# Kernel optimization log

Hardware: AMD Instinct MI355X
Metric: run time of the kernel (lower is better)

Reference implementation:

```python
import jax, jax.numpy as jnp
import numpy as np

T = 8192   # sequence length (sent_len)
D = 512    # word_emb_dim
H = 2048   # enc_lstm_dim
S = 512    # number of segments (len(action_pos))
EPS = 1e-4 # additive constant in the original _masked_softmax denominator


def setup_inputs() -> dict:
    key = jax.random.key(0)
    ks = jax.random.split(key, 16)
    s = 0.02  # small init scale keeps exp() stable
    seg_len = T // S
    action_pos = (jnp.arange(1, S + 1, dtype=jnp.int32) * seg_len - 1)  # last = T-1
    action = jnp.zeros((T,), jnp.int32).at[action_pos].set(1)
    return {
        "sent": jax.random.normal(ks[0], (T, D), jnp.float32),
        "Wi1": jax.random.normal(ks[1], (3 * H, D), jnp.float32) * s,
        "Wh1": jax.random.normal(ks[2], (3 * H, H), jnp.float32) * s,
        "bi1": jax.random.normal(ks[3], (3 * H,), jnp.float32) * s,
        "bh1": jax.random.normal(ks[4], (3 * H,), jnp.float32) * s,
        "Wi2": jax.random.normal(ks[5], (3 * H, H), jnp.float32) * s,
        "Wh2": jax.random.normal(ks[6], (3 * H, H), jnp.float32) * s,
        "bi2": jax.random.normal(ks[7], (3 * H,), jnp.float32) * s,
        "bh2": jax.random.normal(ks[8], (3 * H,), jnp.float32) * s,
        "Wl": jax.random.normal(ks[9], (H, H), jnp.float32) * s,
        "bl": jax.random.normal(ks[10], (H,), jnp.float32) * s,
        "wa": jax.random.normal(ks[11], (H,), jnp.float32) * s,
        "Wl2": jax.random.normal(ks[12], (H, H), jnp.float32) * s,
        "bl2": jax.random.normal(ks[13], (H,), jnp.float32) * s,
        "wa2": jax.random.normal(ks[14], (H,), jnp.float32) * s,
        "action": action,
        "action_pos": action_pos,
    }


def _gru_scan(xs, reset, Wi, Wh, bi, bh):
    """GRU over leading axis; hidden state zeroed after steps where reset==1.
    xs: (N, in), reset: (N,) int. Returns outputs (N, H)."""
    gi_all = xs @ Wi.T + bi  # (N, 3H) precompute input gates as one GEMM

    def step(h, inp):
        gi, a = inp
        gh = Wh @ h + bh
        r = jax.nn.sigmoid(gi[:H] + gh[:H])
        z = jax.nn.sigmoid(gi[H:2 * H] + gh[H:2 * H])
        n = jnp.tanh(gi[2 * H:] + r * gh[2 * H:])
        hn = (1.0 - z) * n + z * h
        h_next = jnp.where(a == 1, jnp.zeros_like(hn), hn)
        return h_next, hn

    h0 = jnp.zeros((H,), xs.dtype)
    _, outs = jax.lax.scan(step, h0, (gi_all, reset))
    return outs


def _degenerate_softmax(a):
    # Original sums exp over a size-1 axis: w = exp(a) / (exp(a) + 1e-4)
    e = jnp.exp(a)
    return e / (e + EPS)


def reference(sent, Wi1, Wh1, bi1, bh1, Wi2, Wh2, bi2, bh2,
              Wl, bl, wa, Wl2, bl2, wa2, action, action_pos):
    # lower GRU with per-step state reset
    outs = _gru_scan(sent, action, Wi1, Wh1, bi1, bh1)          # (T, H)
    emb_h = jnp.tanh(outs @ Wl.T + bl)                           # (T, H)
    w = _degenerate_softmax(emb_h @ wa)                          # (T,)
    weighted = w[:, None] * emb_h                                # (T, H)
    # segment i covers tokens (action_pos[i-1], action_pos[i]]
    seg_id = jnp.searchsorted(action_pos, jnp.arange(T), side='left')
    seg = jax.ops.segment_max(weighted, seg_id, num_segments=S)  # (S, H)
    # upper GRU over segment embeddings (no resets, zero init)
    outs2 = _gru_scan(seg, jnp.zeros((S,), jnp.int32), Wi2, Wh2, bi2, bh2)
    e2 = jnp.tanh(outs2 @ Wl2.T + bl2)                           # (S, H)
    w2 = _degenerate_softmax(e2 @ wa2)                           # (S,)
    emb = jnp.max(w2[:, None] * e2, axis=0, keepdims=True)       # (1, H)
    return emb
```

## Files before the change

kernel.cpp:

```cpp
#include <hip/hip_runtime.h>
#include <stdint.h>

typedef unsigned short u16;
typedef unsigned int u32;
typedef unsigned long long u64;
typedef __attribute__((ext_vector_type(4))) float f32x4;
typedef __attribute__((ext_vector_type(8))) short bf16x8;

constexpr int kT = 8192;
constexpr int kD = 512;
constexpr int kH = 2048;
constexpr int kH3 = 6144;
constexpr int kS = 512;
constexpr int kSeg = 16;
constexpr int kNWG2 = 256;
constexpr int kREP = 8;

__device__ __forceinline__ float bf2f(u16 u) {
  union { float f; u32 u; } v; v.u = ((u32)u) << 16; return v.f;
}
__device__ __forceinline__ u16 f2bf(float f) {
  union { float f; u32 u; } v; v.f = f;
  u32 lsb = (v.u >> 16) & 1u;
  v.u += 0x7fffu + lsb;
  return (u16)(v.u >> 16);
}
__device__ __forceinline__ float bflo(u32 x) {
  union { float f; u32 u; } v; v.u = x << 16; return v.f;
}
__device__ __forceinline__ float bfhi(u32 x) {
  union { float f; u32 u; } v; v.u = x & 0xffff0000u; return v.f;
}
__device__ __forceinline__ float sigm(float x) { return 1.f / (1.f + expf(-x)); }

__device__ __forceinline__ void g2l16(const u16* g, u16* l) {
  __builtin_amdgcn_global_load_lds(
      (const __attribute__((address_space(1))) u32*)g,
      (__attribute__((address_space(3))) u32*)l, 16, 0, 0);
}

__device__ __forceinline__ u64 aload64(const u64* p) {
  return __hip_atomic_load(p, __ATOMIC_RELAXED, __HIP_MEMORY_SCOPE_AGENT);
}
__device__ __forceinline__ void astore64(u64* p, u64 v) {
  __hip_atomic_store(p, v, __ATOMIC_RELAXED, __HIP_MEMORY_SCOPE_AGENT);
}

__global__ void cvt_bf16(const float* __restrict__ in, u16* __restrict__ out, int n4) {
  int i = blockIdx.x * blockDim.x + threadIdx.x;
  if (i >= n4) return;
  const float4 v = *(const float4*)(in + (size_t)i * 4);
  uint2 o;
  o.x = (u32)f2bf(v.x) | ((u32)f2bf(v.y) << 16);
  o.y = (u32)f2bf(v.z) | ((u32)f2bf(v.w) << 16);
  *(uint2*)(out + (size_t)i * 4) = o;
}

template<int EPI>
__global__ __launch_bounds__(256)
void gemm_bt(const u16* __restrict__ A, int lda,
             const u16* __restrict__ B, int ldb,
             u16* __restrict__ Obf, const float* __restrict__ bias,
             int M, int N, int K)
{
  __shared__ u16 ls[4 * 16384];
  const int tid = threadIdx.x;
  const int w = tid >> 6, lane = tid & 63;
  const int wr = w >> 1, wc = w & 1;
  const int arow0 = blockIdx.y * 128;
  const int brow0 = blockIdx.x * 128;
  const int srow = w * 32 + (lane >> 3);
  const int scol = (lane & 7) * 8;
  const u16* gA = A + (size_t)(arow0 + srow) * lda + scol;
  const u16* gB = B + (size_t)(brow0 + srow) * ldb + scol;
  const int sb = w * 32 * 64;

  f32x4 acc[4][4];
#pragma unroll
  for (int m = 0; m < 4; ++m)
#pragma unroll
    for (int n = 0; n < 4; ++n) acc[m][n] = (f32x4)0.f;

  const int fr = lane & 15;
  const int kq = lane >> 4;
  const int nk = K >> 6;

  auto stage = [&](int buf, int kt) {
    u16* la = &ls[buf * 16384 + sb];
    u16* lb = &ls[buf * 16384 + 8192 + sb];
#pragma unroll
    for (int i = 0; i < 4; ++i) g2l16(gA + (size_t)i * 8 * lda + kt, la + i * 8 * 64);
#pragma unroll
    for (int i = 0; i < 4; ++i) g2l16(gB + (size_t)i * 8 * ldb + kt, lb + i * 8 * 64);
  };

  stage(0, 0);
  if (nk > 1) stage(1, 64);
  if (nk > 2) stage(2, 128);

  for (int i = 0; i < nk; ++i) {
    if (i + 2 < nk) asm volatile("s_waitcnt vmcnt(16)" ::: "memory");
    else            asm volatile("s_waitcnt vmcnt(0)" ::: "memory");
    __builtin_amdgcn_s_barrier();
    __builtin_amdgcn_sched_barrier(0);
    if (i + 3 < nk) stage((i + 3) & 3, (i + 3) * 64);
    const u16* lsA = &ls[(i & 3) * 16384];
    const u16* lsB = lsA + 8192;
#pragma unroll
    for (int kk = 0; kk < 2; ++kk) {
      bf16x8 af[4], bq[4];
#pragma unroll
      for (int m = 0; m < 4; ++m)
        af[m] = *(const bf16x8*)&lsA[(wr * 64 + m * 16 + fr) * 64 + kk * 32 + kq * 8];
#pragma unroll
      for (int n = 0; n < 4; ++n)
        bq[n] = *(const bf16x8*)&lsB[(wc * 64 + n * 16 + fr) * 64 + kk * 32 + kq * 8];
#pragma unroll
      for (int m = 0; m < 4; ++m)
#pragma unroll
        for (int n = 0; n < 4; ++n)
          acc[m][n] = __builtin_amdgcn_mfma_f32_16x16x32_bf16(af[m], bq[n], acc[m][n], 0, 0, 0);
    }
  }

#pragma unroll
  for (int m = 0; m < 4; ++m) {
#pragma unroll
    for (int n = 0; n < 4; ++n) {
      const int row0 = arow0 + wr * 64 + m * 16 + kq * 4;
      const int col = brow0 + wc * 64 + n * 16 + fr;
      if (EPI == 1) {
#pragma unroll
        for (int i = 0; i < 4; ++i)
          Obf[(size_t)(row0 + i) * N + col] = f2bf(acc[m][n][i]);
      } else {
        const float bv = bias[col];
#pragma unroll
        for (int i = 0; i < 4; ++i)
          Obf[(size_t)(row0 + i) * N + col] = f2bf(tanhf(acc[m][n][i] + bv));
      }
    }
  }
}

__global__ __launch_bounds__(256) void gru1_gates(
    const u16* __restrict__ gi, const u16* __restrict__ gh,
    const float* __restrict__ bi, const float* __restrict__ bh,
    u16* __restrict__ h_bf, u16* __restrict__ outs_bf, int t)
{
  const int idx = blockIdx.x * 256 + threadIdx.x;
  const int seg = idx >> 10, jp = idx & 1023;
  const u32* gi32 = (const u32*)gi;
  const u32* gh32 = (const u32*)gh;
  const int base = seg * 3072;
  const u32 gir = gi32[base + jp],        ghr = gh32[base + jp];
  const u32 giz = gi32[base + 1024 + jp], ghz = gh32[base + 1024 + jp];
  const u32 gin = gi32[base + 2048 + jp], ghn = gh32[base + 2048 + jp];
  const float2 bir = *(const float2*)&bi[2 * jp];
  const float2 biz = *(const float2*)&bi[kH + 2 * jp];
  const float2 bin = *(const float2*)&bi[2 * kH + 2 * jp];
  const float2 bhr = *(const float2*)&bh[2 * jp];
  const float2 bhz = *(const float2*)&bh[kH + 2 * jp];
  const float2 bhn = *(const float2*)&bh[2 * kH + 2 * jp];
  const u32 hp = ((const u32*)h_bf)[seg * 1024 + jp];
  float hn[2];
#pragma unroll
  for (int e = 0; e < 2; ++e) {
    const float gr = e ? bfhi(gir) : bflo(gir), hr = e ? bfhi(ghr) : bflo(ghr);
    const float gz = e ? bfhi(giz) : bflo(giz), hz = e ? bfhi(ghz) : bflo(ghz);
    const float gn = e ? bfhi(gin) : bflo(gin), hh = e ? bfhi(ghn) : bflo(ghn);
    const float r = sigm(gr + (e ? bir.y : bir.x) + hr + (e ? bhr.y : bhr.x));
    const float z = sigm(gz + (e ? biz.y : biz.x) + hz + (e ? bhz.y : bhz.x));
    const float n = tanhf(gn + (e ? bin.y : bin.x) + r * (hh + (e ? bhn.y : bhn.x)));
    const float hprev = e ? bfhi(hp) : bflo(hp);
    hn[e] = (1.f - z) * n + z * hprev;
  }
  const u32 packed = (u32)f2bf(hn[0]) | ((u32)f2bf(hn[1]) << 16);
  ((u32*)h_bf)[seg * 1024 + jp] = packed;
  ((u32*)outs_bf)[(size_t)(seg * kSeg + t) * 1024 + jp] = packed;
}

__global__ __launch_bounds__(256) void seg_weight_max(
    const u16* __restrict__ embh, const float* __restrict__ wa,
    u16* __restrict__ seg_bf)
{
  __shared__ float wrow[16];
  const int s = blockIdx.x, tid = threadIdx.x;
  const int w = tid >> 6, lane = tid & 63;
#pragma unroll
  for (int rr = 0; rr < 4; ++rr) {
    const int r = w * 4 + rr;
    const u16* row = embh + ((size_t)s * kSeg + r) * kH;
    float p = 0.f;
#pragma unroll
    for (int k = 0; k < 32; ++k) {
      const int c = lane + 64 * k;
      p += bf2f(row[c]) * wa[c];
    }
#pragma unroll
    for (int off = 32; off; off >>= 1) p += __shfl_down(p, off, 64);
    if (lane == 0) { const float e = expf(p); wrow[r] = e / (e + 1e-4f); }
  }
  __syncthreads();
#pragma unroll
  for (int i = 0; i < 8; ++i) {
    const int c = tid + 256 * i;
    float m = -1e30f;
#pragma unroll
    for (int r = 0; r < 16; ++r)
      m = fmaxf(m, wrow[r] * bf2f(embh[((size_t)s * kSeg + r) * kH + c]));
    seg_bf[(size_t)s * kH + c] = f2bf(m);
  }
}

__global__ __launch_bounds__(512)
void gru2_persistent(const u16* __restrict__ Wh2bf, const u16* __restrict__ gi2b,
                     const float* __restrict__ bi2, const float* __restrict__ bh2,
                     u64* __restrict__ hrep,
                     u16* __restrict__ outs2)
{
  __shared__ u16 wl[24 * kH];
  __shared__ u32 hlb[1024];
  __shared__ float gil_all[512 * 24];
  __shared__ float rowsum[24];
  __shared__ alignas(16) u16 hnl[8];
  const int wg = blockIdx.x, tid = threadIdx.x;
  const int g0 = wg * 8;
  const int grp = wg & 7;
  uint4* wl4 = (uint4*)wl;
  for (int i = tid; i < 24 * 256; i += 512) {
    const int lr = i >> 8, q = i & 255;
    const int grow = (lr >> 3) * kH + g0 + (lr & 7);
    wl4[i] = ((const uint4*)Wh2bf)[(size_t)grow * 256 + q];
  }
  for (int i = tid; i < 512 * 24; i += 512) {
    const int t = i / 24, idx = i - t * 24;
    gil_all[i] = bf2f(gi2b[(size_t)t * kH3 + (idx >> 3) * kH + g0 + (idx & 7)]);
  }
  float bir = 0, biz = 0, bin = 0, bhr = 0, bhz = 0, bhn = 0;
  if (tid < 8) {
    const int jj = g0 + tid;
    bir = bi2[jj]; biz = bi2[kH + jj]; bin = bi2[2 * kH + jj];
    bhr = bh2[jj]; bhz = bh2[kH + jj]; bhn = bh2[2 * kH + jj];
  }
  const int w = tid >> 6, lane = tid & 63;
  const uint4* hl4 = (const uint4*)hlb;

  for (int t = 0; t < 512; ++t) {
    const u64* hs = hrep + ((size_t)(t & 1) * kREP + grp) * 1024;
    u64 v0, v1;
    for (;;) {
      v0 = aload64(&hs[2 * tid]);
      if ((u32)(v0 >> 32) >= (u32)t) break;
      __builtin_amdgcn_s_sleep(1);
    }
    for (;;) {
      v1 = aload64(&hs[2 * tid + 1]);
      if ((u32)(v1 >> 32) >= (u32)t) break;
      __builtin_amdgcn_s_sleep(1);
    }
    hlb[2 * tid] = (u32)v0;
    hlb[2 * tid + 1] = (u32)v1;
    __syncthreads();
#pragma unroll
    for (int rr = 0; rr < 3; ++rr) {
      const int lr = w * 3 + rr;
      float p = 0.f;
#pragma unroll
      for (int k = 0; k < 4; ++k) {
        const int q = lane + 64 * k;
        const uint4 wv = wl4[lr * 256 + q];
        const uint4 hv = hl4[q];
        p += bflo(wv.x) * bflo(hv.x) + bfhi(wv.x) * bfhi(hv.x);
        p += bflo(wv.y) * bflo(hv.y) + bfhi(wv.y) * bfhi(hv.y);
        p += bflo(wv.z) * bflo(hv.z) + bfhi(wv.z) * bfhi(hv.z);
        p += bflo(wv.w) * bflo(hv.w) + bfhi(wv.w) * bfhi(hv.w);
      }
#pragma unroll
      for (int off = 32; off; off >>= 1) p += __shfl_down(p, off, 64);
      if (lane == 0) rowsum[lr] = p;
    }
    __syncthreads();
    if (tid < 8) {
      const float r = sigm(gil_all[t * 24 + tid] + bir + rowsum[tid] + bhr);
      const float z = sigm(gil_all[t * 24 + 8 + tid] + biz + rowsum[8 + tid] + bhz);
      const float n = tanhf(gil_all[t * 24 + 16 + tid] + bin +
                            r * (rowsum[16 + tid] + bhn));
      const u32 hw = hlb[(g0 + tid) >> 1];
      const float hprev = (tid & 1) ? bfhi(hw) : bflo(hw);
      hnl[tid] = f2bf((1.f - z) * n + z * hprev);
    }
    __syncthreads();
    if (tid < 4 * kREP) {
      const int rep = tid >> 2, k = tid & 3;
      const u64 val = ((u64)(u32)(t + 1) << 32) | ((const u32*)hnl)[k];
      astore64(&hrep[((size_t)((t + 1) & 1) * kREP + rep) * 1024 + wg * 4 + k], val);
    }
    if (tid == 0)
      *(uint4*)&outs2[(size_t)t * kH + g0] = *(const uint4*)hnl;
  }
}

__global__ void calc_w2(const u16* __restrict__ e2, const float* __restrict__ wa2,
                        float* __restrict__ w2) {
  const int s = blockIdx.x, lane = threadIdx.x;
  float p = 0.f;
#pragma unroll
  for (int k = 0; k < 32; ++k) {
    const int c = lane + 64 * k;
    p += bf2f(e2[(size_t)s * kH + c]) * wa2[c];
  }
#pragma unroll
  for (int off = 32; off; off >>= 1) p += __shfl_down(p, off, 64);
  if (lane == 0) { const float e = expf(p); w2[s] = e / (e + 1e-4f); }
}

__global__ void final_max(const u16* __restrict__ e2, const float* __restrict__ w2,
                          float* __restrict__ out) {
  const int j = blockIdx.x * blockDim.x + threadIdx.x;
  float m = -1e30f;
  for (int s = 0; s < 512; ++s)
    m = fmaxf(m, w2[s] * bf2f(e2[(size_t)s * kH + j]));
  out[j] = m;
}

extern "C" void kernel_launch(void* const* d_in, const int* in_sizes, int n_in,
                              void* d_out, int out_size, void* d_ws, size_t ws_size,
                              hipStream_t stream)
{
  (void)in_sizes; (void)n_in; (void)out_size; (void)ws_size;
  const float* sent = (const float*)d_in[0];
  const float* Wi1f = (const float*)d_in[1];
  const float* Wh1f = (const float*)d_in[2];
  const float* bi1  = (const float*)d_in[3];
  const float* bh1  = (const float*)d_in[4];
  const float* Wi2f = (const float*)d_in[5];
  const float* Wh2f = (const float*)d_in[6];
  const float* bi2  = (const float*)d_in[7];
  const float* bh2  = (const float*)d_in[8];
  const float* Wlf  = (const float*)d_in[9];
  const float* bl   = (const float*)d_in[10];
  const float* wa   = (const float*)d_in[11];
  const float* Wl2f = (const float*)d_in[12];
  const float* bl2  = (const float*)d_in[13];
  const float* wa2  = (const float*)d_in[14];
  float* out = (float*)d_out;

  char* base = (char*)d_ws;
  size_t off = 0;
  auto alloc = [&](size_t b) { char* p = base + off; off += (b + 255) & ~(size_t)255; return p; };
  u16* sent_bf = (u16*)alloc((size_t)kT * kD * 2);
  u16* Wi1b    = (u16*)alloc((size_t)kH3 * kD * 2);
  u16* Wh1b    = (u16*)alloc((size_t)kH3 * kH * 2);
  u16* Wi2b    = (u16*)alloc((size_t)kH3 * kH * 2);
  u16* Wh2b    = (u16*)alloc((size_t)kH3 * kH * 2);
  u16* Wlb     = (u16*)alloc((size_t)kH * kH * 2);
  u16* Wl2b    = (u16*)alloc((size_t)kH * kH * 2);
  u16* gi_buf  = (u16*)alloc((size_t)kS * kH3 * 2);
  u16* gh_buf  = (u16*)alloc((size_t)kS * kH3 * 2);
  u16* h1b     = (u16*)alloc((size_t)kS * kH * 2);
  u16* outs_bf = (u16*)alloc((size_t)kT * kH * 2);
  u16* seg_bf  = (u16*)alloc((size_t)kS * kH * 2);
  u64* hrep    = (u64*)alloc((size_t)2 * kREP * 1024 * 8);
  u16* outs2   = (u16*)alloc((size_t)kS * kH * 2);
  u16* e2b     = (u16*)alloc((size_t)kS * kH * 2);
  float* w2    = (float*)alloc(kS * 4);
  u16* embh = sent_bf;
  u16* gi2b = gi_buf;

  hipMemsetAsync(h1b, 0, (size_t)kS * kH * 2, stream);
  hipMemsetAsync(hrep, 0, (size_t)2 * kREP * 1024 * 8, stream);

  auto cvt = [&](const float* src, u16* dst, int n) {
    const int n4 = n / 4;
    cvt_bf16<<<dim3((n4 + 255) / 256), dim3(256), 0, stream>>>(src, dst, n4);
  };
  cvt(sent, sent_bf, kT * kD);
  cvt(Wi1f, Wi1b, kH3 * kD);
  cvt(Wh1f, Wh1b, kH3 * kH);
  cvt(Wi2f, Wi2b, kH3 * kH);
  cvt(Wh2f, Wh2b, kH3 * kH);
  cvt(Wlf, Wlb, kH * kH);
  cvt(Wl2f, Wl2b, kH * kH);

  for (int t = 0; t < kSeg; ++t) {
    gemm_bt<1><<<dim3(kH3 / 128, kS / 128), dim3(256), 0, stream>>>(
        h1b, kH, Wh1b, kH, gh_buf, nullptr, kS, kH3, kH);
    gemm_bt<1><<<dim3(kH3 / 128, kS / 128), dim3(256), 0, stream>>>(
        sent_bf + t * kD, kSeg * kD, Wi1b, kD, gi_buf, nullptr, kS, kH3, kD);
    gru1_gates<<<dim3(kS * kH / 512), dim3(256), 0, stream>>>(
        gi_buf, gh_buf, bi1, bh1, h1b, outs_bf, t);
  }
  gemm_bt<2><<<dim3(kH / 128, kT / 128), dim3(256), 0, stream>>>(
      outs_bf, kH, Wlb, kH, embh, bl, kT, kH, kH);
  seg_weight_max<<<dim3(kS), dim3(256), 0, stream>>>(embh, wa, seg_bf);
  gemm_bt<1><<<dim3(kH3 / 128, kS / 128), dim3(256), 0, stream>>>(
      seg_bf, kH, Wi2b, kH, gi2b, nullptr, kS, kH3, kH);
  gru2_persistent<<<dim3(kNWG2), dim3(512), 0, stream>>>(
      Wh2b, gi2b, bi2, bh2, hrep, outs2);
  gemm_bt<2><<<dim3(kH / 128, kS / 128), dim3(256), 0, stream>>>(
      outs2, kH, Wl2b, kH, e2b, bl2, kS, kH, kH);
  calc_w2<<<dim3(kS), dim3(64), 0, stream>>>(e2b, wa2, w2);
  final_max<<<dim3(kH / 256), dim3(256), 0, stream>>>(e2b, w2, out);
}
```

Baseline: 2.958 ms.

## Tag each bf16 hidden value per word and poll with cache-bypassing 16-byte loads

Reworks the inter-workgroup hidden-state exchange in the persistent upper GRU. Each bf16 value is now packed with a 16-bit step tag in its own 32-bit word, so a thread polls one 16-byte load with sc0/sc1 cache bypass and a wave-wide any() instead of two 64-bit atomic loads. Replicas drop from 8 to 4, which halves the broadcast stores per step. This aims to cut per-step synchronisation latency on the serial 512-step recurrence, but relies on 16-byte stores being seen atomically per dword and on inline asm memory semantics.

```diff
diff --git a/kernel.cpp b/kernel.cpp
--- a/kernel.cpp
+++ b/kernel.cpp
@@ -6,6 +6,7 @@
 typedef unsigned long long u64;
 typedef __attribute__((ext_vector_type(4))) float f32x4;
 typedef __attribute__((ext_vector_type(8))) short bf16x8;
+typedef __attribute__((ext_vector_type(4))) u32 u32x4;
 
 constexpr int kT = 8192;
 constexpr int kD = 512;
@@ -14,7 +15,7 @@
 constexpr int kS = 512;
 constexpr int kSeg = 16;
 constexpr int kNWG2 = 256;
-constexpr int kREP = 8;
+constexpr int kREP = 4;
 
 __device__ __forceinline__ float bf2f(u16 u) {
   union { float f; u32 u; } v; v.u = ((u32)u) << 16; return v.f;
@@ -39,11 +40,14 @@
       (__attribute__((address_space(3))) u32*)l, 16, 0, 0);
 }
 
-__device__ __forceinline__ u64 aload64(const u64* p) {
-  return __hip_atomic_load(p, __ATOMIC_RELAXED, __HIP_MEMORY_SCOPE_AGENT);
-}
-__device__ __forceinline__ void astore64(u64* p, u64 v) {
-  __hip_atomic_store(p, v, __ATOMIC_RELAXED, __HIP_MEMORY_SCOPE_AGENT);
+__device__ __forceinline__ u32x4 bypass_load16(const u32* p) {
+  u32x4 v;
+  asm volatile("global_load_dwordx4 %0, %1, off sc0 sc1\n\ts_waitcnt vmcnt(0)"
+               : "=&v"(v) : "v"(p) : "memory");
+  return v;
+}
+__device__ __forceinline__ void bypass_store16(u32* p, u32x4 v) {
+  asm volatile("global_store_dwordx4 %0, %1, off sc0 sc1" :: "v"(p), "v"(v) : "memory");
 }
 
 __global__ void cvt_bf16(const float* __restrict__ in, u16* __restrict__ out, int n4) {
@@ -216,7 +220,7 @@
 __global__ __launch_bounds__(512)
 void gru2_persistent(const u16* __restrict__ Wh2bf, const u16* __restrict__ gi2b,
                      const float* __restrict__ bi2, const float* __restrict__ bh2,
-                     u64* __restrict__ hrep,
+                     u32* __restrict__ hx,
                      u16* __restrict__ outs2)
 {
   __shared__ u16 wl[24 * kH];
@@ -226,7 +230,7 @@
   __shared__ alignas(16) u16 hnl[8];
   const int wg = blockIdx.x, tid = threadIdx.x;
   const int g0 = wg * 8;
-  const int grp = wg & 7;
+  const int rep = wg & (kREP - 1);
   uint4* wl4 = (uint4*)wl;
   for (int i = tid; i < 24 * 256; i += 512) {
     const int lr = i >> 8, q = i & 255;
@@ -247,38 +251,35 @@
   const uint4* hl4 = (const uint4*)hlb;
 
   for (int t = 0; t < 512; ++t) {
-    const u64* hs = hrep + ((size_t)(t & 1) * kREP + grp) * 1024;
-    u64 v0, v1;
+    const u32 want = (u32)t & 0xffffu;
+    const u32* p = hx + ((size_t)(t & 1) * kREP + rep) * 2048 + 4 * tid;
+    u32x4 v;
     for (;;) {
-      v0 = aload64(&hs[2 * tid]);
-      if ((u32)(v0 >> 32) >= (u32)t) break;
+      v = bypass_load16(p);
+      const u32 bad = ((v.x ^ want) | (v.y ^ want) | (v.z ^ want) | (v.w ^ want)) & 0xffffu;
+      if (!__any((int)bad)) break;
       __builtin_amdgcn_s_sleep(1);
     }
-    for (;;) {
-      v1 = aload64(&hs[2 * tid + 1]);
-      if ((u32)(v1 >> 32) >= (u32)t) break;
-      __builtin_amdgcn_s_sleep(1);
-    }
-    hlb[2 * tid] = (u32)v0;
-    hlb[2 * tid + 1] = (u32)v1;
+    hlb[2 * tid]     = (v.x >> 16) | (v.y & 0xffff0000u);
+    hlb[2 * tid + 1] = (v.z >> 16) | (v.w & 0xffff0000u);
     __syncthreads();
 #pragma unroll
     for (int rr = 0; rr < 3; ++rr) {
       const int lr = w * 3 + rr;
-      float p = 0.f;
+      float p2 = 0.f;
 #pragma unroll
       for (int k = 0; k < 4; ++k) {
         const int q = lane + 64 * k;
         const uint4 wv = wl4[lr * 256 + q];
         const uint4 hv = hl4[q];
-        p += bflo(wv.x) * bflo(hv.x) + bfhi(wv.x) * bfhi(hv.x);
-        p += bflo(wv.y) * bflo(hv.y) + bfhi(wv.y) * bfhi(hv.y);
-        p += bflo(wv.z) * bflo(hv.z) + bfhi(wv.z) * bfhi(hv.z);
-        p += bflo(wv.w) * bflo(hv.w) + bfhi(wv.w) * bfhi(hv.w);
+        p2 += bflo(wv.x) * bflo(hv.x) + bfhi(wv.x) * bfhi(hv.x);
+        p2 += bflo(wv.y) * bflo(hv.y) + bfhi(wv.y) * bfhi(hv.y);
+        p2 += bflo(wv.z) * bflo(hv.z) + bfhi(wv.z) * bfhi(hv.z);
+        p2 += bflo(wv.w) * bflo(hv.w) + bfhi(wv.w) * bfhi(hv.w);
       }
 #pragma unroll
-      for (int off = 32; off; off >>= 1) p += __shfl_down(p, off, 64);
-      if (lane == 0) rowsum[lr] = p;
+      for (int off = 32; off; off >>= 1) p2 += __shfl_down(p2, off, 64);
+      if (lane == 0) rowsum[lr] = p2;
     }
     __syncthreads();
     if (tid < 8) {
@@ -291,10 +292,17 @@
       hnl[tid] = f2bf((1.f - z) * n + z * hprev);
     }
     __syncthreads();
-    if (tid < 4 * kREP) {
-      const int rep = tid >> 2, k = tid & 3;
-      const u64 val = ((u64)(u32)(t + 1) << 32) | ((const u32*)hnl)[k];
-      astore64(&hrep[((size_t)((t + 1) & 1) * kREP + rep) * 1024 + wg * 4 + k], val);
+    if (tid < 2 * kREP) {
+      const int orep = tid >> 1, half = tid & 1;
+      const u16* h4 = hnl + half * 4;
+      const u32 tagv = (u32)(t + 1) & 0xffffu;
+      u32x4 m;
+      m.x = ((u32)h4[0] << 16) | tagv;
+      m.y = ((u32)h4[1] << 16) | tagv;
+      m.z = ((u32)h4[2] << 16) | tagv;
+      m.w = ((u32)h4[3] << 16) | tagv;
+      u32* q = hx + ((size_t)((t + 1) & 1) * kREP + orep) * 2048 + wg * 8 + half * 4;
+      bypass_store16(q, m);
     }
     if (tid == 0)
       *(uint4*)&outs2[(size_t)t * kH + g0] = *(const uint4*)hnl;
@@ -361,15 +369,15 @@
   u16* h1b     = (u16*)alloc((size_t)kS * kH * 2);
   u16* outs_bf = (u16*)alloc((size_t)kT * kH * 2);
   u16* seg_bf  = (u16*)alloc((size_t)kS * kH * 2);
-  u64* hrep    = (u64*)alloc((size_t)2 * kREP * 1024 * 8);
+  u32* hx      = (u32*)alloc((size_t)2 * kREP * 2048 * 4);
   u16* outs2   = (u16*)alloc((size_t)kS * kH * 2);
   u16* e2b     = (u16*)alloc((size_t)kS * kH * 2);
   float* w2    = (float*)alloc(kS * 4);
   u16* embh = sent_bf;
   u16* gi2b = gi_buf;
 
-  hipMemsetAsync(h1b, 0, (size_t)kS * kH * 2, stream);
-  hipMemsetAsync(hrep, 0, (size_t)2 * kREP * 1024 * 8, stream);
+  (void)hipMemsetAsync(h1b, 0, (size_t)kS * kH * 2, stream);
+  (void)hipMemsetAsync(hx, 0, (size_t)2 * kREP * 2048 * 4, stream);
 
   auto cvt = [&](const float* src, u16* dst, int n) {
     const int n4 = n / 4;
@@ -379,9 +387,9 @@
   cvt(Wi1f, Wi1b, kH3 * kD);
   cvt(Wh1f, Wh1b, kH3 * kH);
   cvt(Wi2f, Wi2b, kH3 * kH);
-  cvt(Wh2f, Wh2b, kH3 * kH);
   cvt(Wlf, Wlb, kH * kH);
   cvt(Wl2f, Wl2b, kH * kH);
+  cvt(Wh2f, Wh2b, kH3 * kH);
 
   for (int t = 0; t < kSeg; ++t) {
     gemm_bt<1><<<dim3(kH3 / 128, kS / 128), dim3(256), 0, stream>>>(
@@ -397,7 +405,7 @@
   gemm_bt<1><<<dim3(kH3 / 128, kS / 128), dim3(256), 0, stream>>>(
       seg_bf, kH, Wi2b, kH, gi2b, nullptr, kS, kH3, kH);
   gru2_persistent<<<dim3(kNWG2), dim3(512), 0, stream>>>(
-      Wh2b, gi2b, bi2, bh2, hrep, outs2);
+      Wh2b, gi2b, bi2, bh2, hx, outs2);
   gemm_bt<2><<<dim3(kH / 128, kS / 128), dim3(256), 0, stream>>>(
       outs2, kH, Wl2b, kH, e2b, bl2, kS, kH, kH);
   calc_w2<<<dim3(kS), dim3(64), 0, stream>>>(e2b, wa2, w2);
```

After: 2.979 ms. About the same (+0.7%).
